# Kernel optimization log

Measured on AMD Instinct MI355X. Metric: run time of the kernel, lower is better.

## Reference

```python
import jax, jax.numpy as jnp
import numpy as np

NBINS = 51
BIN_WIDTH = 2.0 / (NBINS - 1)
BS, D = 1024, 128
N_CLASSES = 32


def setup_inputs() -> dict:
    key = jax.random.key(0)
    kx, kl = jax.random.split(key)
    x = jax.random.normal(kx, (BS, D), dtype=jnp.float32)
    x = x / jnp.linalg.norm(x, axis=1, keepdims=True)  # similarities in [-1, 1]
    labels = jax.random.randint(kl, (BS,), 0, N_CLASSES, dtype=jnp.int64)
    return {"x": x, "labels": labels}


def reference(x, labels):
    # Pairwise similarities of upper-triangular (i < j) pairs.
    sim = x @ x.T                                   # [bs, bs]
    bs = x.shape[0]
    iu, ju = jnp.triu_indices(bs, k=1)              # n_pairs indices
    s = sim[iu, ju]                                 # [n_pairs]
    pos = labels[iu] == labels[ju]                  # [n_pairs] bool

    # Soft (linear) binning: pair with sim s assigned bin value v = floor((s+1)/bw)*bw - 1
    # contributes (v+bw-s)/bw to bin b and (s-v)/bw to bin b+1 (triangular kernel),
    # exactly matching the original indsa/indsb masking scheme.
    b = jnp.floor((s + 1.0) / BIN_WIDTH).astype(jnp.int32)  # bin index in [0, nbins-1]
    v = b.astype(s.dtype) * BIN_WIDTH - 1.0                  # assigned bin value
    w_lo = (v + BIN_WIDTH - s) / BIN_WIDTH                   # weight for bin b
    w_hi = (s - v) / BIN_WIDTH                               # weight for bin b+1
    b_hi = jnp.clip(b + 1, 0, NBINS - 1)                     # w_hi == 0 when clipped

    def hist(mask):
        m = mask.astype(s.dtype)
        h = jnp.zeros((NBINS,), s.dtype)
        h = h.at[b].add(w_lo * m)
        h = h.at[b_hi].add(w_hi * m)
        return h / m.sum()

    hist_pos = hist(pos)
    hist_neg = hist(~pos)

    # CDF of positive histogram, then histogram loss.
    hist_pos_cdf = jnp.cumsum(hist_pos)
    return jnp.sum(hist_neg * hist_pos_cdf)
```

## Files before the change

kernel.cpp:

```cpp
#include <hip/hip_runtime.h>

#define NBINS 51
#define NT    32
#define TILE  32
#define DV4   32
#define NBLK  (NT * (NT + 1) / 2)
#define NCOPY 16
#define HSTR  103

__global__ __launch_bounds__(256) void pair_hist_kernel(
    const float* __restrict__ x,
    const int*   __restrict__ labels,
    float*       __restrict__ ghist)
{
    __shared__ float4 As[TILE][DV4];
    __shared__ float4 Bs[TILE][DV4];
    __shared__ int    la[TILE], lb[TILE];
    __shared__ float  shist[NCOPY * HSTR];

    int rem = blockIdx.x;
    int bi = 0;
    while (rem >= NT - bi) { rem -= NT - bi; ++bi; }
    const int bj = bi + rem;

    const int t = threadIdx.x;
    for (int k = t; k < NCOPY * HSTR; k += 256) shist[k] = 0.0f;

    const float4* xv = (const float4*)x;
    #pragma unroll
    for (int k = 0; k < 4; ++k) {
        int e = t + 256 * k;
        int r = e >> 5;
        int c = e & 31;
        int sw = c ^ ((r >> 1) & 7);
        As[r][sw] = xv[(bi * TILE + r) * DV4 + c];
        Bs[r][sw] = xv[(bj * TILE + r) * DV4 + c];
    }
    if (t < TILE) {
        la[t] = labels[bi * TILE + t];
        lb[t] = labels[bj * TILE + t];
    }
    __syncthreads();

    const int tx = t & 15;
    const int ty = t >> 4;
    const int i0 = ty * 2, j0 = tx * 2;
    const int kA = ty & 7;
    const int kB = tx & 7;

    float acc00 = 0.f, acc01 = 0.f, acc10 = 0.f, acc11 = 0.f;
    #pragma unroll 4
    for (int d4 = 0; d4 < DV4; ++d4) {
        float4 a0 = As[i0    ][d4 ^ kA];
        float4 a1 = As[i0 + 1][d4 ^ kA];
        float4 b0 = Bs[j0    ][d4 ^ kB];
        float4 b1 = Bs[j0 + 1][d4 ^ kB];
        acc00 += a0.x*b0.x + a0.y*b0.y + a0.z*b0.z + a0.w*b0.w;
        acc01 += a0.x*b1.x + a0.y*b1.y + a0.z*b1.z + a0.w*b1.w;
        acc10 += a1.x*b0.x + a1.y*b0.y + a1.z*b0.z + a1.w*b0.w;
        acc11 += a1.x*b1.x + a1.y*b1.y + a1.z*b1.z + a1.w*b1.w;
    }

    const float BW = 2.0f / (NBINS - 1);
    float accs[2][2] = {{acc00, acc01}, {acc10, acc11}};
    float* myh = &shist[(t & (NCOPY - 1)) * HSTR];

    #pragma unroll
    for (int r = 0; r < 2; ++r) {
        #pragma unroll
        for (int c = 0; c < 2; ++c) {
            int gi = bi * TILE + i0 + r;
            int gj = bj * TILE + j0 + c;
            if (gi < gj) {
                float s = accs[r][c];
                int b = (int)floorf((s + 1.0f) / BW);
                b = min(max(b, 0), NBINS - 1);
                float v = (float)b * BW - 1.0f;
                float wlo = (v + BW - s) / BW;
                float whi = (s - v) / BW;
                int bh = min(b + 1, NBINS - 1);
                int base = (la[i0 + r] == lb[j0 + c]) ? 0 : NBINS;
                unsafeAtomicAdd(&myh[base + b],  wlo);
                unsafeAtomicAdd(&myh[base + bh], whi);
            }
        }
    }

    __syncthreads();
    if (t < 2 * NBINS) {
        float s = 0.f;
        #pragma unroll
        for (int c = 0; c < NCOPY; ++c) s += shist[c * HSTR + t];
        unsafeAtomicAdd(&ghist[t], s);
    }
}

__global__ void finalize_kernel(const float* __restrict__ gh,
                                float* __restrict__ out)
{
    int t = threadIdx.x;
    float hp = (t < NBINS) ? gh[t]         : 0.0f;
    float hn = (t < NBINS) ? gh[NBINS + t] : 0.0f;

    float sp = hp, sn = hn;
    #pragma unroll
    for (int off = 32; off > 0; off >>= 1) {
        sp += __shfl_xor(sp, off, 64);
        sn += __shfl_xor(sn, off, 64);
    }

    float cdf = hp;
    #pragma unroll
    for (int off = 1; off < 64; off <<= 1) {
        float v = __shfl_up(cdf, off, 64);
        if (t >= off) cdf += v;
    }

    float contrib = hn * cdf;
    #pragma unroll
    for (int off = 32; off > 0; off >>= 1)
        contrib += __shfl_xor(contrib, off, 64);

    if (t == 0) out[0] = contrib / (sp * sn);
}

extern "C" void kernel_launch(void* const* d_in, const int* in_sizes, int n_in,
                              void* d_out, int out_size, void* d_ws, size_t ws_size,
                              hipStream_t stream)
{
    const float* x      = (const float*)d_in[0];
    const int*   labels = (const int*)d_in[1];
    float*       ghist  = (float*)d_ws;

    hipMemsetAsync(ghist, 0, 2 * NBINS * sizeof(float), stream);
    pair_hist_kernel<<<NBLK, 256, 0, stream>>>(x, labels, ghist);
    finalize_kernel<<<1, 64, 0, stream>>>(ghist, (float*)d_out);
}
```

Measured before the change: 78.11 us.

## Replace global atomic histogram merge with per-block partials and finalize reduction

Each block now writes its 102-bin partial histogram to its own slot in workspace instead of atomically adding into a shared global histogram. The finalize kernel, launched with 1024 threads, reduces the 528 partials in two stages through shared memory. This drops the memset launch and the contention on global atomics. In exchange the final reduction runs on a single block and reads about 215 KB, and it needs more workspace.

Result: faster. 75.79 us (-3.0%).

```diff
diff --git a/kernel.cpp b/kernel.cpp
--- a/kernel.cpp
+++ b/kernel.cpp
@@ -7,11 +7,12 @@
 #define NBLK  (NT * (NT + 1) / 2)
 #define NCOPY 16
 #define HSTR  103
+#define NH    (2 * NBINS)
 
 __global__ __launch_bounds__(256) void pair_hist_kernel(
     const float* __restrict__ x,
     const int*   __restrict__ labels,
-    float*       __restrict__ ghist)
+    float*       __restrict__ gpart)
 {
     __shared__ float4 As[TILE][DV4];
     __shared__ float4 Bs[TILE][DV4];
@@ -87,41 +88,67 @@
     }
 
     __syncthreads();
-    if (t < 2 * NBINS) {
+    if (t < NH) {
         float s = 0.f;
         #pragma unroll
         for (int c = 0; c < NCOPY; ++c) s += shist[c * HSTR + t];
-        unsafeAtomicAdd(&ghist[t], s);
+        gpart[blockIdx.x * NH + t] = s;
     }
 }
 
-__global__ void finalize_kernel(const float* __restrict__ gh,
-                                float* __restrict__ out)
+__global__ __launch_bounds__(1024) void finalize_kernel(
+    const float* __restrict__ gpart,
+    float*       __restrict__ out)
 {
-    int t = threadIdx.x;
-    float hp = (t < NBINS) ? gh[t]         : 0.0f;
-    float hn = (t < NBINS) ? gh[NBINS + t] : 0.0f;
+    __shared__ float red[10][NH];
+    __shared__ float tot[NH];
 
-    float sp = hp, sn = hn;
-    #pragma unroll
-    for (int off = 32; off > 0; off >>= 1) {
-        sp += __shfl_xor(sp, off, 64);
-        sn += __shfl_xor(sn, off, 64);
+    const int t = threadIdx.x;
+    const int p = t / NH;
+    const int b = t - p * NH;
+
+    if (t < 10 * NH) {
+        float s = 0.f;
+        #pragma unroll 4
+        for (int blk = p; blk < NBLK; blk += 10)
+            s += gpart[blk * NH + b];
+        red[p][b] = s;
     }
+    __syncthreads();
 
-    float cdf = hp;
-    #pragma unroll
-    for (int off = 1; off < 64; off <<= 1) {
-        float v = __shfl_up(cdf, off, 64);
-        if (t >= off) cdf += v;
+    if (t < NH) {
+        float s = 0.f;
+        #pragma unroll
+        for (int q = 0; q < 10; ++q) s += red[q][t];
+        tot[t] = s;
     }
+    __syncthreads();
 
-    float contrib = hn * cdf;
-    #pragma unroll
-    for (int off = 32; off > 0; off >>= 1)
-        contrib += __shfl_xor(contrib, off, 64);
+    if (t < 64) {
+        float hp = (t < NBINS) ? tot[t]         : 0.0f;
+        float hn = (t < NBINS) ? tot[NBINS + t] : 0.0f;
 
-    if (t == 0) out[0] = contrib / (sp * sn);
+        float sp = hp, sn = hn;
+        #pragma unroll
+        for (int off = 32; off > 0; off >>= 1) {
+            sp += __shfl_xor(sp, off, 64);
+            sn += __shfl_xor(sn, off, 64);
+        }
+
+        float cdf = hp;
+        #pragma unroll
+        for (int off = 1; off < 64; off <<= 1) {
+            float v = __shfl_up(cdf, off, 64);
+            if (t >= off) cdf += v;
+        }
+
+        float contrib = hn * cdf;
+        #pragma unroll
+        for (int off = 32; off > 0; off >>= 1)
+            contrib += __shfl_xor(contrib, off, 64);
+
+        if (t == 0) out[0] = contrib / (sp * sn);
+    }
 }
 
 extern "C" void kernel_launch(void* const* d_in, const int* in_sizes, int n_in,
@@ -130,9 +157,8 @@
 {
     const float* x      = (const float*)d_in[0];
     const int*   labels = (const int*)d_in[1];
-    float*       ghist  = (float*)d_ws;
+    float*       gpart  = (float*)d_ws;
 
-    hipMemsetAsync(ghist, 0, 2 * NBINS * sizeof(float), stream);
-    pair_hist_kernel<<<NBLK, 256, 0, stream>>>(x, labels, ghist);
-    finalize_kernel<<<1, 64, 0, stream>>>(ghist, (float*)d_out);
+    pair_hist_kernel<<<NBLK, 256, 0, stream>>>(x, labels, gpart);
+    finalize_kernel<<<1, 1024, 0, stream>>>(gpart, (float*)d_out);
 }
```
